# Kernel tuning notes

Hardware: AMD Instinct MI355X
Metric: run time of the kernel (lower is better)

Reference implementation:

```python
import jax, jax.numpy as jnp
import numpy as np

B = 8192
DIMS_IN = (8, 8, 16)    # prod = 1024 = dim_in
DIMS_OUT = (16, 16, 16) # prod = 4096 = dim_out
RANK = 64


def setup_inputs() -> dict:
    key = jax.random.key(0)
    k0, k1, k2, k3 = jax.random.split(key, 4)
    x = jax.random.normal(k0, (B, 1024), dtype=jnp.float32)
    # TT-cores: [r_prev, d_in, d_out, r_next], init scale randn/sqrt(r_prev), last core *0.02
    g1 = jax.random.normal(k1, (1, 8, 16, RANK), dtype=jnp.float32)
    g2 = jax.random.normal(k2, (RANK, 8, 16, RANK), dtype=jnp.float32) / np.sqrt(RANK).astype(np.float32)
    g3 = jax.random.normal(k3, (RANK, 16, 16, 1), dtype=jnp.float32) * (0.02 / np.sqrt(RANK).astype(np.float32))
    return {"x": x, "g1": g1, "g2": g2, "g3": g3}


def reference(x, g1, g2, g3):
    # x: [B, dim_in] -> [B, i1, i2, i3]
    xr = x.reshape((x.shape[0],) + DIMS_IN)
    # TT-matrix contraction chain: sum over ranks (w,r,s,z; w=z=1) and input modes (i,j,k)
    # g1[w,i,p,r], g2[r,j,q,s], g3[s,k,m,z], x[b,i,j,k] -> y[b,p,q,m]
    y = jnp.einsum('wipr,rjqs,skmz,bijk->bpqm', g1, g2, g3, xr)
    return y.reshape(x.shape[0], -1)  # [B, dim_out]
```

## Files before the change

### kernel.cpp

```cpp
#include <hip/hip_runtime.h>


#define K_DIM  1024
#define N_DIM  4096

typedef __bf16 bf16x8 __attribute__((ext_vector_type(8)));
typedef float  f32x4  __attribute__((ext_vector_type(4)));

__device__ __forceinline__ unsigned int f2bf(float f) {
    unsigned int x = __float_as_uint(f);
    return (x + 0x7FFFu + ((x >> 16) & 1u)) >> 16;
}

__device__ __forceinline__ void barx() {
    asm volatile("" ::: "memory");
    __builtin_amdgcn_s_barrier();
    asm volatile("" ::: "memory");
}

__device__ __forceinline__ void stage16(const ushort* src, const ushort* dst) {
    __builtin_amdgcn_global_load_lds(
        (const __attribute__((address_space(1))) void*)src,
        (__attribute__((address_space(3))) void*)dst, 16, 0, 0);
}

__global__ __launch_bounds__(256) void mergeW(const float* __restrict__ g1,
                                              const float* __restrict__ g2,
                                              const float* __restrict__ g3,
                                              ushort* __restrict__ Wt) {
    __shared__ float g1s[512];
    __shared__ float S[4096];
    __shared__ float g3s[16384];
    const int t = threadIdx.x;
    const int p = blockIdx.x >> 4, q = blockIdx.x & 15;

    for (int u = t; u < 512; u += 256) {
        int i = u >> 6, r = u & 63;
        g1s[u] = g1[(i * 16 + p) * 64 + r];
    }
    for (int u = t; u < 4096; u += 256) {
        int m4 = u & 3, sk = u >> 2, k = sk & 15;
        float4 v = ((const float4*)g3)[u];
        ((float4*)g3s)[sk * 4 + (m4 ^ ((k >> 1) & 3))] = v;
    }
    __syncthreads();

    for (int u = t; u < 512; u += 256) {
        int jj = u >> 6, ss = u & 63;
        float acc[8] = {};
        const float* g2p = g2 + (jj * 16 + q) * 64 + ss;
#pragma unroll 8
        for (int r = 0; r < 64; ++r) {
            float v = g2p[r * 8192];
#pragma unroll
            for (int i = 0; i < 8; ++i) acc[i] += g1s[i * 64 + r] * v;
        }
        float4* Sp = (float4*)&S[u * 8];
        Sp[0] = make_float4(acc[0], acc[1], acc[2], acc[3]);
        Sp[1] = make_float4(acc[4], acc[5], acc[6], acc[7]);
    }
    __syncthreads();

    const int pq = p * 16 + q;
#pragma unroll
    for (int c = 0; c < 4; ++c) {
        int kin = c * 256 + t;
        int i = kin >> 7, j = (kin >> 4) & 7, k = kin & 15;
        float acc[16] = {};
        for (int s = 0; s < 64; ++s) {
            float a = S[(j * 64 + s) * 8 + i];
            const float4* g3v = (const float4*)&g3s[(s * 16 + k) * 16];
#pragma unroll
            for (int m4 = 0; m4 < 4; ++m4) {
                float4 v = g3v[m4 ^ ((k >> 1) & 3)];
                acc[m4 * 4 + 0] += a * v.x;
                acc[m4 * 4 + 1] += a * v.y;
                acc[m4 * 4 + 2] += a * v.z;
                acc[m4 * 4 + 3] += a * v.w;
            }
        }
#pragma unroll
        for (int m = 0; m < 16; ++m)
            Wt[(size_t)(pq * 16 + m) * K_DIM + kin] = (ushort)f2bf(acc[m]);
    }
}

__global__ __launch_bounds__(256) void castx(const float* __restrict__ x,
                                             ushort* __restrict__ Xb) {
    size_t o = (size_t)blockIdx.x * 256 + threadIdx.x;
    const float4* xp = (const float4*)(x + o * 8);
    float4 v0 = xp[0], v1 = xp[1];
    uint4 out;
    out.x = f2bf(v0.x) | (f2bf(v0.y) << 16);
    out.y = f2bf(v0.z) | (f2bf(v0.w) << 16);
    out.z = f2bf(v1.x) | (f2bf(v1.y) << 16);
    out.w = f2bf(v1.z) | (f2bf(v1.w) << 16);
    *(uint4*)(Xb + o * 8) = out;
}

#define MF(mm, nn, aa, bb) acc[mm][nn] = __builtin_amdgcn_mfma_f32_16x16x32_bf16(aa, bb, acc[mm][nn], 0, 0, 0)

__global__ __launch_bounds__(512, 2) void gemm_bf16(const ushort* __restrict__ Xb,
                                                    const ushort* __restrict__ Wt,
                                                    float* __restrict__ C) {
    __shared__ ushort lds[65536];

    const int t = threadIdx.x;
    const int w = t >> 6, l = t & 63;
    const int wr = w >> 2, wc = w & 3;
    const int fr = l & 15, cc = l >> 4;

    const int bid = blockIdx.x;
    const int swz = (bid & 7) * 64 + (bid >> 3);
    const int tileM = (swz >> 4) * 256;
    const int tileN = (swz & 15) * 256;

    int offA[8], offB[4];
#pragma unroll
    for (int m = 0; m < 8; ++m) {
        int R = wr * 128 + m * 16 + fr;
        offA[m] = (R * 32 + ((cc ^ ((R >> 1) & 3)) * 8)) * 2;
    }
#pragma unroll
    for (int n = 0; n < 4; ++n) {
        int R = wc * 64 + n * 16 + fr;
        offB[n] = (8192 + R * 32 + ((cc ^ ((R >> 1) & 3)) * 8)) * 2;
    }

    const ushort* srcA[2]; const ushort* srcB[2];
    int dstAoff[2], dstBoff[2];
#pragma unroll
    for (int j = 0; j < 2; ++j) {
        int s = j * 512 + t;
        int r = s >> 2, pch = s & 3;
        int cs = pch ^ ((r >> 1) & 3);
        srcA[j] = Xb + (size_t)(tileM + r) * K_DIM + cs * 8;
        srcB[j] = Wt + (size_t)(tileN + r) * K_DIM + cs * 8;
        dstAoff[j] = j * 4096 + w * 512;
        dstBoff[j] = 8192 + j * 4096 + w * 512;
    }

    f32x4 acc[8][4] = {};

#pragma unroll
    for (int pt = 0; pt < 3; ++pt) {
        ushort* sl = lds + pt * 16384;
        const int ko = pt * 32;
        stage16(srcA[0] + ko, sl + dstAoff[0]);
        stage16(srcA[1] + ko, sl + dstAoff[1]);
        stage16(srcB[0] + ko, sl + dstBoff[0]);
        stage16(srcB[1] + ko, sl + dstBoff[1]);
    }
    asm volatile("s_waitcnt vmcnt(8)" ::: "memory");
    barx();

#pragma unroll 4
    for (int kt = 0; kt < 32; ++kt) {
        const char* slb = (const char*)(lds + (kt & 3) * 16384);
        ushort* ssl = lds + ((kt + 3) & 3) * 16384;
        int kst = kt + 3; if (kst > 31) kst = 0;
        const int ko = kst * 32;

        stage16(srcA[0] + ko, ssl + dstAoff[0]);
        stage16(srcA[1] + ko, ssl + dstAoff[1]);
        stage16(srcB[0] + ko, ssl + dstBoff[0]);
        stage16(srcB[1] + ko, ssl + dstBoff[1]);

        bf16x8 a0 = *(const bf16x8*)(slb + offA[0]);
        bf16x8 a1 = *(const bf16x8*)(slb + offA[1]);
        bf16x8 a2 = *(const bf16x8*)(slb + offA[2]);
        bf16x8 a3 = *(const bf16x8*)(slb + offA[3]);
        bf16x8 b0 = *(const bf16x8*)(slb + offB[0]);
        bf16x8 b1 = *(const bf16x8*)(slb + offB[1]);
        bf16x8 b2 = *(const bf16x8*)(slb + offB[2]);
        bf16x8 b3 = *(const bf16x8*)(slb + offB[3]);
        bf16x8 a4 = *(const bf16x8*)(slb + offA[4]);
        bf16x8 a5 = *(const bf16x8*)(slb + offA[5]);
        bf16x8 a6 = *(const bf16x8*)(slb + offA[6]);
        bf16x8 a7 = *(const bf16x8*)(slb + offA[7]);

        __builtin_amdgcn_s_setprio(1);
        MF(0,0,a0,b0); MF(0,1,a0,b1); MF(0,2,a0,b2); MF(0,3,a0,b3);
        MF(1,0,a1,b0); MF(1,1,a1,b1); MF(1,2,a1,b2); MF(1,3,a1,b3);
        MF(2,0,a2,b0); MF(2,1,a2,b1); MF(2,2,a2,b2); MF(2,3,a2,b3);
        MF(3,0,a3,b0); MF(3,1,a3,b1); MF(3,2,a3,b2); MF(3,3,a3,b3);
        MF(4,0,a4,b0); MF(4,1,a4,b1); MF(4,2,a4,b2); MF(4,3,a4,b3);
        MF(5,0,a5,b0); MF(5,1,a5,b1); MF(5,2,a5,b2); MF(5,3,a5,b3);
        MF(6,0,a6,b0); MF(6,1,a6,b1); MF(6,2,a6,b2); MF(6,3,a6,b3);
        MF(7,0,a7,b0); MF(7,1,a7,b1); MF(7,2,a7,b2); MF(7,3,a7,b3);
        __builtin_amdgcn_s_setprio(0);

        asm volatile("s_waitcnt vmcnt(8)" ::: "memory");
        barx();
    }
    asm volatile("s_waitcnt vmcnt(0)" ::: "memory");

    const int cr = (l >> 4) * 4;
#pragma unroll
    for (int m = 0; m < 8; ++m) {
        const int row0 = tileM + wr * 128 + m * 16 + cr;
#pragma unroll
        for (int n = 0; n < 4; ++n) {
            const int col = tileN + wc * 64 + n * 16 + fr;
            float* Cp = C + (size_t)row0 * N_DIM + col;
#pragma unroll
            for (int r = 0; r < 4; ++r)
                Cp[(size_t)r * N_DIM] = acc[m][n][r];
        }
    }
}

extern "C" void kernel_launch(void* const* d_in, const int* in_sizes, int n_in,
                              void* d_out, int out_size, void* d_ws, size_t ws_size,
                              hipStream_t stream) {
    const float* x  = (const float*)d_in[0];
    const float* g1 = (const float*)d_in[1];
    const float* g2 = (const float*)d_in[2];
    const float* g3 = (const float*)d_in[3];
    float* out = (float*)d_out;

    char* ws = (char*)d_ws;
    ushort* Wt = (ushort*)ws;
    ushort* Xb = (ushort*)(ws + (8u << 20));

    mergeW<<<256, 256, 0, stream>>>(g1, g2, g3, Wt);
    castx <<<4096, 256, 0, stream>>>(x, Xb);
    gemm_bf16<<<512, 512, 0, stream>>>(Xb, Wt, out);
}
```

Baseline: 254.1 us.

## Pre-pack operands into MFMA fragment layout and load GEMM fragments directly from global

```diff
diff --git a/kernel.cpp b/kernel.cpp
--- a/kernel.cpp
+++ b/kernel.cpp
@@ -12,22 +12,10 @@
     return (x + 0x7FFFu + ((x >> 16) & 1u)) >> 16;
 }
 
-__device__ __forceinline__ void barx() {
-    asm volatile("" ::: "memory");
-    __builtin_amdgcn_s_barrier();
-    asm volatile("" ::: "memory");
-}
-
-__device__ __forceinline__ void stage16(const ushort* src, const ushort* dst) {
-    __builtin_amdgcn_global_load_lds(
-        (const __attribute__((address_space(1))) void*)src,
-        (__attribute__((address_space(3))) void*)dst, 16, 0, 0);
-}
-
 __global__ __launch_bounds__(256) void mergeW(const float* __restrict__ g1,
                                               const float* __restrict__ g2,
                                               const float* __restrict__ g3,
-                                              ushort* __restrict__ Wt) {
+                                              ushort* __restrict__ WtF) {
     __shared__ float g1s[512];
     __shared__ float S[4096];
     __shared__ float g3s[16384];
@@ -79,107 +67,70 @@
                 acc[m4 * 4 + 3] += a * v.w;
             }
         }
+        size_t base = ((size_t)pq * 128 + (kin >> 3)) * 128 + (kin & 7);
 #pragma unroll
         for (int m = 0; m < 16; ++m)
-            Wt[(size_t)(pq * 16 + m) * K_DIM + kin] = (ushort)f2bf(acc[m]);
+            WtF[base + m * 8] = (ushort)f2bf(acc[m]);
     }
 }
 
-__global__ __launch_bounds__(256) void castx(const float* __restrict__ x,
-                                             ushort* __restrict__ Xb) {
-    size_t o = (size_t)blockIdx.x * 256 + threadIdx.x;
-    const float4* xp = (const float4*)(x + o * 8);
+__global__ __launch_bounds__(256) void packA(const float* __restrict__ x,
+                                             ushort* __restrict__ XbF) {
+    int o = blockIdx.x * 256 + threadIdx.x;
+    int kc = o & 127, row = o >> 7;
+    const float4* xp = (const float4*)(x + (size_t)row * K_DIM + kc * 8);
     float4 v0 = xp[0], v1 = xp[1];
-    uint4 out;
-    out.x = f2bf(v0.x) | (f2bf(v0.y) << 16);
-    out.y = f2bf(v0.z) | (f2bf(v0.w) << 16);
-    out.z = f2bf(v1.x) | (f2bf(v1.y) << 16);
-    out.w = f2bf(v1.z) | (f2bf(v1.w) << 16);
-    *(uint4*)(Xb + o * 8) = out;
+    uint4 outv;
+    outv.x = f2bf(v0.x) | (f2bf(v0.y) << 16);
+    outv.y = f2bf(v0.z) | (f2bf(v0.w) << 16);
+    outv.z = f2bf(v1.x) | (f2bf(v1.y) << 16);
+    outv.w = f2bf(v1.z) | (f2bf(v1.w) << 16);
+    *(uint4*)(XbF + (((size_t)(row >> 4) * 128 + kc) * 16 + (row & 15)) * 8) = outv;
 }
 
 #define MF(mm, nn, aa, bb) acc[mm][nn] = __builtin_amdgcn_mfma_f32_16x16x32_bf16(aa, bb, acc[mm][nn], 0, 0, 0)
 
-__global__ __launch_bounds__(512, 2) void gemm_bf16(const ushort* __restrict__ Xb,
-                                                    const ushort* __restrict__ Wt,
-                                                    float* __restrict__ C) {
-    __shared__ ushort lds[65536];
-
+__global__ __launch_bounds__(512, 2) void gemm_direct(const ushort* __restrict__ XbF,
+                                                      const ushort* __restrict__ WtF,
+                                                      float* __restrict__ C) {
     const int t = threadIdx.x;
     const int w = t >> 6, l = t & 63;
     const int wr = w >> 2, wc = w & 3;
-    const int fr = l & 15, cc = l >> 4;
+    const int fr = l & 15;
 
     const int bid = blockIdx.x;
     const int swz = (bid & 7) * 64 + (bid >> 3);
     const int tileM = (swz >> 4) * 256;
     const int tileN = (swz & 15) * 256;
 
-    int offA[8], offB[4];
+    const int mb0 = (tileM >> 4) + wr * 8;
+    const int nb0 = (tileN >> 4) + wc * 4;
+
+    const ushort* Ap[8];
+    const ushort* Bp[4];
 #pragma unroll
-    for (int m = 0; m < 8; ++m) {
-        int R = wr * 128 + m * 16 + fr;
-        offA[m] = (R * 32 + ((cc ^ ((R >> 1) & 3)) * 8)) * 2;
-    }
+    for (int m = 0; m < 8; ++m) Ap[m] = XbF + (size_t)(mb0 + m) * 16384 + l * 8;
 #pragma unroll
-    for (int n = 0; n < 4; ++n) {
-        int R = wc * 64 + n * 16 + fr;
-        offB[n] = (8192 + R * 32 + ((cc ^ ((R >> 1) & 3)) * 8)) * 2;
-    }
-
-    const ushort* srcA[2]; const ushort* srcB[2];
-    int dstAoff[2], dstBoff[2];
-#pragma unroll
-    for (int j = 0; j < 2; ++j) {
-        int s = j * 512 + t;
-        int r = s >> 2, pch = s & 3;
-        int cs = pch ^ ((r >> 1) & 3);
-        srcA[j] = Xb + (size_t)(tileM + r) * K_DIM + cs * 8;
-        srcB[j] = Wt + (size_t)(tileN + r) * K_DIM + cs * 8;
-        dstAoff[j] = j * 4096 + w * 512;
-        dstBoff[j] = 8192 + j * 4096 + w * 512;
-    }
+    for (int n = 0; n < 4; ++n) Bp[n] = WtF + (size_t)(nb0 + n) * 16384 + l * 8;
 
     f32x4 acc[8][4] = {};
 
-#pragma unroll
-    for (int pt = 0; pt < 3; ++pt) {
-        ushort* sl = lds + pt * 16384;
-        const int ko = pt * 32;
-        stage16(srcA[0] + ko, sl + dstAoff[0]);
-        stage16(srcA[1] + ko, sl + dstAoff[1]);
-        stage16(srcB[0] + ko, sl + dstBoff[0]);
-        stage16(srcB[1] + ko, sl + dstBoff[1]);
-    }
-    asm volatile("s_waitcnt vmcnt(8)" ::: "memory");
-    barx();
+#pragma unroll 2
+    for (int kt = 0; kt < 32; ++kt) {
+        const int ko = kt * 512;
+        bf16x8 b0 = *(const bf16x8*)(Bp[0] + ko);
+        bf16x8 b1 = *(const bf16x8*)(Bp[1] + ko);
+        bf16x8 b2 = *(const bf16x8*)(Bp[2] + ko);
+        bf16x8 b3 = *(const bf16x8*)(Bp[3] + ko);
+        bf16x8 a0 = *(const bf16x8*)(Ap[0] + ko);
+        bf16x8 a1 = *(const bf16x8*)(Ap[1] + ko);
+        bf16x8 a2 = *(const bf16x8*)(Ap[2] + ko);
+        bf16x8 a3 = *(const bf16x8*)(Ap[3] + ko);
+        bf16x8 a4 = *(const bf16x8*)(Ap[4] + ko);
+        bf16x8 a5 = *(const bf16x8*)(Ap[5] + ko);
+        bf16x8 a6 = *(const bf16x8*)(Ap[6] + ko);
+        bf16x8 a7 = *(const bf16x8*)(Ap[7] + ko);
 
-#pragma unroll 4
-    for (int kt = 0; kt < 32; ++kt) {
-        const char* slb = (const char*)(lds + (kt & 3) * 16384);
-        ushort* ssl = lds + ((kt + 3) & 3) * 16384;
-        int kst = kt + 3; if (kst > 31) kst = 0;
-        const int ko = kst * 32;
-
-        stage16(srcA[0] + ko, ssl + dstAoff[0]);
-        stage16(srcA[1] + ko, ssl + dstAoff[1]);
-        stage16(srcB[0] + ko, ssl + dstBoff[0]);
-        stage16(srcB[1] + ko, ssl + dstBoff[1]);
-
-        bf16x8 a0 = *(const bf16x8*)(slb + offA[0]);
-        bf16x8 a1 = *(const bf16x8*)(slb + offA[1]);
-        bf16x8 a2 = *(const bf16x8*)(slb + offA[2]);
-        bf16x8 a3 = *(const bf16x8*)(slb + offA[3]);
-        bf16x8 b0 = *(const bf16x8*)(slb + offB[0]);
-        bf16x8 b1 = *(const bf16x8*)(slb + offB[1]);
-        bf16x8 b2 = *(const bf16x8*)(slb + offB[2]);
-        bf16x8 b3 = *(const bf16x8*)(slb + offB[3]);
-        bf16x8 a4 = *(const bf16x8*)(slb + offA[4]);
-        bf16x8 a5 = *(const bf16x8*)(slb + offA[5]);
-        bf16x8 a6 = *(const bf16x8*)(slb + offA[6]);
-        bf16x8 a7 = *(const bf16x8*)(slb + offA[7]);
-
-        __builtin_amdgcn_s_setprio(1);
         MF(0,0,a0,b0); MF(0,1,a0,b1); MF(0,2,a0,b2); MF(0,3,a0,b3);
         MF(1,0,a1,b0); MF(1,1,a1,b1); MF(1,2,a1,b2); MF(1,3,a1,b3);
         MF(2,0,a2,b0); MF(2,1,a2,b1); MF(2,2,a2,b2); MF(2,3,a2,b3);
@@ -188,12 +139,7 @@
         MF(5,0,a5,b0); MF(5,1,a5,b1); MF(5,2,a5,b2); MF(5,3,a5,b3);
         MF(6,0,a6,b0); MF(6,1,a6,b1); MF(6,2,a6,b2); MF(6,3,a6,b3);
         MF(7,0,a7,b0); MF(7,1,a7,b1); MF(7,2,a7,b2); MF(7,3,a7,b3);
-        __builtin_amdgcn_s_setprio(0);
-
-        asm volatile("s_waitcnt vmcnt(8)" ::: "memory");
-        barx();
     }
-    asm volatile("s_waitcnt vmcnt(0)" ::: "memory");
 
     const int cr = (l >> 4) * 4;
 #pragma unroll
@@ -220,10 +166,10 @@
     float* out = (float*)d_out;
 
     char* ws = (char*)d_ws;
-    ushort* Wt = (ushort*)ws;
-    ushort* Xb = (ushort*)(ws + (8u << 20));
+    ushort* WtF = (ushort*)ws;
+    ushort* XbF = (ushort*)(ws + (8u << 20));
 
-    mergeW<<<256, 256, 0, stream>>>(g1, g2, g3, Wt);
-    castx <<<4096, 256, 0, stream>>>(x, Xb);
-    gemm_bf16<<<512, 512, 0, stream>>>(Xb, Wt, out);
+    mergeW<<<256, 256, 0, stream>>>(g1, g2, g3, WtF);
+    packA <<<4096, 256, 0, stream>>>(x, XbF);
+    gemm_direct<<<512, 512, 0, stream>>>(XbF, WtF, out);
 }
```

Result: slower. 283.4 us (+11.5%).
